# Kernel optimization log

Hardware: AMD Instinct MI355X
Metric: run time of the kernel (lower is better)

## Reference

```python
import jax, jax.numpy as jnp
import numpy as np

B, S, D, H = 4, 2048, 1024, 16
HD = D // H
BITS = 8
LEVELS = 2 ** BITS - 1          # number of negative log2 levels
SCALING = 32.0 / 16.0           # lora alpha / rank for 8-bit adapter
NEG_INF = -1e9


def log_fake_quant(x, reduce_axes):
    """Per-channel log-domain fake quantization with straight-through estimator.
    Scale = per-channel max-abs; magnitudes snapped to power-of-two fractions of scale."""
    s = jnp.maximum(jnp.max(jnp.abs(x), axis=reduce_axes, keepdims=True), 1e-8)
    ratio = jnp.clip(jnp.abs(x) / s, 2.0 ** (-LEVELS), 1.0)
    e = jnp.round(jnp.log2(ratio))                      # in [-LEVELS, 0]
    q = jnp.sign(x) * s * jnp.exp2(e)
    return x + jax.lax.stop_gradient(q - x)             # STE


def cpt_linear(x, W, b, lA, lB):
    """CPTLinear: fake-quantized activation/weight GEMM + bias + LoRA on the fp input."""
    xq = log_fake_quant(x, tuple(range(x.ndim - 1)))     # per last-dim channel
    Wq = log_fake_quant(W, (1,))                         # per output row (channel_dim=0)
    out = xq @ Wq.T + b
    return out + (x @ lA @ lB) * SCALING


def setup_inputs() -> dict:
    key = jax.random.key(0)
    ks = jax.random.split(key, 8)
    causal = jnp.tril(jnp.ones((S, S), dtype=bool))
    mask = jnp.where(causal, 0.0, NEG_INF).astype(jnp.float32)[None, None]  # [1,1,S,S]
    return {
        "hidden_states": jax.random.normal(ks[0], (B, S, D), jnp.float32),
        "attention_mask": mask,
        "W_attn": jax.random.normal(ks[1], (3 * D, D), jnp.float32) * 0.02,
        "b_attn": jnp.zeros((3 * D,), jnp.float32),
        "lA_attn": jax.random.normal(ks[2], (D, 16), jnp.float32) * 0.01,
        "lB_attn": jax.random.normal(ks[3], (16, 3 * D), jnp.float32) * 0.01,
        "W_proj": jax.random.normal(ks[4], (D, D), jnp.float32) * 0.02,
        "b_proj": jnp.zeros((D,), jnp.float32),
        "lA_proj": jax.random.normal(ks[5], (D, 16), jnp.float32) * 0.01,
        "lB_proj": jax.random.normal(ks[6], (16, D), jnp.float32) * 0.01,
    }


def reference(hidden_states, attention_mask, W_attn, b_attn, lA_attn, lB_attn,
              W_proj, b_proj, lA_proj, lB_proj):
    qkv = cpt_linear(hidden_states, W_attn, b_attn, lA_attn, lB_attn)  # [B,S,3D]
    q, k, v = jnp.split(qkv, 3, axis=-1)

    def to_heads(t):
        return t.reshape(B, S, H, HD).transpose(0, 2, 1, 3)            # [B,H,S,HD]

    q, k, v = to_heads(q), to_heads(k), to_heads(v)
    scores = jnp.einsum("bhqd,bhkd->bhqk", q, k) / np.float32(np.sqrt(HD))
    scores = scores + attention_mask
    attn = jax.nn.softmax(scores, axis=-1)                             # dropout: eval mode (identity)
    out = jnp.einsum("bhqk,bhkd->bhqd", attn, v)
    out = out.transpose(0, 2, 1, 3).reshape(B, S, D)
    return cpt_linear(out, W_proj, b_proj, lA_proj, lB_proj)
```

## Files before the change

kernel.cpp:

```cpp
#include <hip/hip_runtime.h>

#define SS 2048
#define DD 1024
#define DQKV 3072
#define KP 1088
#define NT64 17
#define MTOT 8192
#define QKSZ ((size_t)MTOT * DD)

typedef unsigned short us;
typedef __attribute__((ext_vector_type(8))) short bf16x8;
typedef __attribute__((ext_vector_type(4))) float f32x4;
typedef __attribute__((ext_vector_type(4))) unsigned u32x4;

#define WAITVM(N) asm volatile("s_waitcnt vmcnt(" #N ")" ::: "memory")
#define WAITLGKM0 asm volatile("s_waitcnt lgkmcnt(0)" ::: "memory")

__device__ __forceinline__ us f2bf(float f) {
    unsigned u = __float_as_uint(f);
    return (us)((u + 0x7fffu + ((u >> 16) & 1u)) >> 16);
}
__device__ __forceinline__ float bf2f(us h) { return __uint_as_float(((unsigned)h) << 16); }
__device__ __forceinline__ void split2(float q, us& h, us& l) {
    h = f2bf(q); l = f2bf(q - bf2f(h));
}
__device__ __forceinline__ unsigned cvtpk(float lo, float hi) {
    unsigned r;
    asm("v_cvt_pk_bf16_f32 %0, %1, %2" : "=v"(r) : "v"(lo), "v"(hi));
    return r;
}

__device__ __forceinline__ int logq_e(float ax, float s) {
    int e = 0;
    if (ax < s) {
        double r = (double)ax / (double)s;
        int ex;
        double mant = frexp(r, &ex);
        e = (mant >= 0.70710678118654752440) ? ex : ex - 1;
        e = (e < -255) ? -255 : e;
    }
    return e;
}
__device__ __forceinline__ float logq_exact(float x, float s) {
    float ax = fabsf(x);
    if (ax == 0.f) return copysignf(0.f, x);
    return copysignf(ldexpf(s, logq_e(ax, s)), x);
}

__device__ __forceinline__ void gll16(const void* g, void* l) {
    __builtin_amdgcn_global_load_lds(
        (const __attribute__((address_space(1))) void*)g,
        (__attribute__((address_space(3))) void*)l, 16, 0, 0);
}


__global__ void k_zero(unsigned* p, int n) {
    int i = blockIdx.x * 256 + threadIdx.x;
    if (i < n) p[i] = 0u;
}

__global__ void k_colmax(const float* __restrict__ x, unsigned* __restrict__ smax) {
    int c = blockIdx.x * 256 + threadIdx.x;
    int r0 = blockIdx.y * 128;
    float m = 0.f;
    for (int r = 0; r < 128; ++r) m = fmaxf(m, fabsf(x[(size_t)(r0 + r) * DD + c]));
    atomicMax(smax + c, __float_as_uint(m));
}

__global__ void k_quant_rows(const float* __restrict__ x, const unsigned* __restrict__ smax,
                             us* __restrict__ xq) {
    int m = blockIdx.x, tx = threadIdx.x;
    float4 xv = ((const float4*)(x + (size_t)m * DD))[tx];
    int c = tx * 4;
    float vv[4] = {xv.x, xv.y, xv.z, xv.w};
    ushort4 qh;
    us* ph = (us*)&qh;
#pragma unroll
    for (int j = 0; j < 4; ++j) {
        float s = fmaxf(__uint_as_float(smax[c + j]), 1e-8f);
        float sh = bf2f(f2bf(s));
        float ax = fabsf(vv[j]);
        if (ax == 0.f) ph[j] = (us)((__float_as_uint(vv[j]) >> 16) & 0x8000u);
        else ph[j] = f2bf(copysignf(ldexpf(sh, logq_e(ax, s)), vv[j]));
    }
    *(ushort4*)(xq + (size_t)m * KP + c) = qh;
    if (tx == 0) xq[(size_t)m * KP + 1056] = 0x3F80;
    else if (tx < 32) xq[(size_t)m * KP + 1056 + tx] = 0;
}

__global__ void k_lora_x(const float* __restrict__ x, const float* __restrict__ lA,
                         us* __restrict__ xq) {
    int w = threadIdx.x >> 6, lane = threadIdx.x & 63;
    int m = blockIdx.x * 4 + w;
    const float* xr = x + (size_t)m * DD;
    float acc[16];
#pragma unroll
    for (int r = 0; r < 16; ++r) acc[r] = 0.f;
#pragma unroll
    for (int i = 0; i < 4; ++i) {
        int c0 = i * 256 + lane * 4;
        float4 xv = *(const float4*)(xr + c0);
        float xs4[4] = {xv.x, xv.y, xv.z, xv.w};
#pragma unroll
        for (int j = 0; j < 4; ++j) {
            float xs = xs4[j];
            const float4* lr = (const float4*)(lA + (size_t)(c0 + j) * 16);
            float4 a0 = lr[0], a1 = lr[1], a2 = lr[2], a3 = lr[3];
            acc[0] += xs * a0.x; acc[1] += xs * a0.y; acc[2] += xs * a0.z; acc[3] += xs * a0.w;
            acc[4] += xs * a1.x; acc[5] += xs * a1.y; acc[6] += xs * a1.z; acc[7] += xs * a1.w;
            acc[8] += xs * a2.x; acc[9] += xs * a2.y; acc[10] += xs * a2.z; acc[11] += xs * a2.w;
            acc[12] += xs * a3.x; acc[13] += xs * a3.y; acc[14] += xs * a3.z; acc[15] += xs * a3.w;
        }
    }
#pragma unroll
    for (int msk = 1; msk < 64; msk <<= 1)
#pragma unroll
        for (int r = 0; r < 16; ++r) acc[r] += __shfl_xor(acc[r], msk);
    if (lane == 0) {
#pragma unroll
        for (int r = 0; r < 16; ++r) {
            us h, l; split2(2.0f * acc[r], h, l);
            xq[(size_t)m * KP + 1024 + r] = h;
            xq[(size_t)m * KP + 1040 + r] = l;
        }
    }
}

__global__ __launch_bounds__(256) void k_quant_w(const float* __restrict__ W, const float* __restrict__ lB,
                                                 const float* __restrict__ bias,
                                                 const unsigned* __restrict__ smax,
                                                 us* __restrict__ wh, us* __restrict__ wl, int Nn) {
    __shared__ float red[4];
    int n = blockIdx.x, tx = threadIdx.x;
    int lane = tx & 63, w = tx >> 6;
    float4 wv = ((const float4*)(W + (size_t)n * DD))[tx];
    float m4 = fmaxf(fmaxf(fabsf(wv.x), fabsf(wv.y)), fmaxf(fabsf(wv.z), fabsf(wv.w)));
#pragma unroll
    for (int msk = 1; msk < 64; msk <<= 1) m4 = fmaxf(m4, __shfl_xor(m4, msk));
    if (lane == 0) red[w] = m4;
    __syncthreads();
    float t = fmaxf(fmaxf(fmaxf(red[0], red[1]), fmaxf(red[2], red[3])), 1e-8f);
    float vv[4] = {wv.x, wv.y, wv.z, wv.w};
    int c = tx * 4;
    ushort4 qh, ql;
    us* ph = (us*)&qh; us* pl = (us*)&ql;
#pragma unroll
    for (int j = 0; j < 4; ++j) {
        float s = fmaxf(__uint_as_float(smax[c + j]), 1e-8f);
        float sh = bf2f(f2bf(s));
        float rho = (s - sh) / sh;
        float q = logq_exact(vv[j], t);
        float wp = q + q * rho;
        split2(wp, ph[j], pl[j]);
    }
    *(ushort4*)(wh + (size_t)n * KP + c) = qh;
    *(ushort4*)(wl + (size_t)n * KP + c) = ql;
    if (tx < 64) {
        us h = 0, l = 0;
        if (tx < 32) { int r = tx & 15; split2(lB[(size_t)r * Nn + n], h, l); }
        else if (tx == 32) split2(bias[n], h, l);
        wh[(size_t)n * KP + 1024 + tx] = h;
        wl[(size_t)n * KP + 1024 + tx] = l;
    }
}


template <int MODE>
__global__ __launch_bounds__(512, 2) void k_gemm(const us* __restrict__ Aq_,
                                                 const us* __restrict__ Bh_, const us* __restrict__ Bl_,
                                                 float* __restrict__ C, int Nn,
                                                 us* __restrict__ Khg, us* __restrict__ Klg,
                                                 float* __restrict__ vbuf) {
    __shared__ us LA[2][16384];
    __shared__ us LBh[2][8192];
    __shared__ us LBl[2][8192];
    int tid = threadIdx.x;
    int bm = blockIdx.x, bn = blockIdx.y;
    int lane = tid & 63, w = tid >> 6;
    int wm = w >> 2, wn = w & 3;
    int l15 = lane & 15, l4 = lane >> 4;
    int srow = tid >> 3;
    int gsrc = ((tid & 7) ^ (srow & 7)) * 8;
    const us* aP  = Aq_ + (size_t)(bm * 256 + srow) * KP + gsrc;
    const us* bhP = Bh_ + (size_t)(bn * 128 + srow) * KP + gsrc;
    const us* blP = Bl_ + (size_t)(bn * 128 + srow) * KP + gsrc;
    f32x4 zero4 = {0.f, 0.f, 0.f, 0.f};
    f32x4 acc[8][2];
#pragma unroll
    for (int i = 0; i < 8; ++i) { acc[i][0] = zero4; acc[i][1] = zero4; }

#define GSTAGE(buf, kt)                                               \
    do {                                                              \
        int k0_ = (kt) * 64;                                          \
        gll16(aP + k0_,                    &LA[(buf)][0]     + tid * 8); \
        gll16(aP + (size_t)64  * KP + k0_, &LA[(buf)][4096]  + tid * 8); \
        gll16(aP + (size_t)128 * KP + k0_, &LA[(buf)][8192]  + tid * 8); \
        gll16(aP + (size_t)192 * KP + k0_, &LA[(buf)][12288] + tid * 8); \
        gll16(bhP + k0_,                   &LBh[(buf)][0]    + tid * 8); \
        gll16(bhP + (size_t)64 * KP + k0_, &LBh[(buf)][4096] + tid * 8); \
        gll16(blP + k0_,                   &LBl[(buf)][0]    + tid * 8); \
        gll16(blP + (size_t)64 * KP + k0_, &LBl[(buf)][4096] + tid * 8); \
    } while (0)

    GSTAGE(0, 0);
    GSTAGE(1, 1);
    WAITVM(8);
    __builtin_amdgcn_s_barrier();
    __builtin_amdgcn_sched_barrier(0);

    int gsw0 = ((l4)     ^ (l15 & 7)) * 8;
    int gsw1 = ((4 + l4) ^ (l15 & 7)) * 8;
    int cur = 0;
    for (int kt = 0; kt < NT64; ++kt) {
        const us* A0  = &LA[cur][0];
        const us* Bh0 = &LBh[cur][0];
        const us* Bl0 = &LBl[cur][0];
        bf16x8 a0[8], b0h[2], b0l[2];
#pragma unroll
        for (int i = 0; i < 8; ++i)
            a0[i] = *(const bf16x8*)(A0 + (wm * 128 + i * 16 + l15) * 64 + gsw0);
#pragma unroll
        for (int i = 0; i < 2; ++i) {
            b0h[i] = *(const bf16x8*)(Bh0 + (wn * 32 + i * 16 + l15) * 64 + gsw0);
            b0l[i] = *(const bf16x8*)(Bl0 + (wn * 32 + i * 16 + l15) * 64 + gsw0);
        }
        __builtin_amdgcn_s_setprio(1);
#pragma unroll
        for (int mi = 0; mi < 8; ++mi)
#pragma unroll
            for (int ni = 0; ni < 2; ++ni) {
                acc[mi][ni] = __builtin_amdgcn_mfma_f32_16x16x32_bf16(a0[mi], b0h[ni], acc[mi][ni], 0, 0, 0);
                acc[mi][ni] = __builtin_amdgcn_mfma_f32_16x16x32_bf16(a0[mi], b0l[ni], acc[mi][ni], 0, 0, 0);
            }
        __builtin_amdgcn_s_setprio(0);
        bf16x8 a1[8], b1h[2], b1l[2];
#pragma unroll
        for (int i = 0; i < 8; ++i)
            a1[i] = *(const bf16x8*)(A0 + (wm * 128 + i * 16 + l15) * 64 + gsw1);
#pragma unroll
        for (int i = 0; i < 2; ++i) {
            b1h[i] = *(const bf16x8*)(Bh0 + (wn * 32 + i * 16 + l15) * 64 + gsw1);
            b1l[i] = *(const bf16x8*)(Bl0 + (wn * 32 + i * 16 + l15) * 64 + gsw1);
        }
        WAITLGKM0;
        __builtin_amdgcn_sched_barrier(0);
        __builtin_amdgcn_s_barrier();
        __builtin_amdgcn_sched_barrier(0);
        if (kt + 2 < NT64) GSTAGE(cur, kt + 2);
        __builtin_amdgcn_s_setprio(1);
#pragma unroll
        for (int mi = 0; mi < 8; ++mi)
#pragma unroll
            for (int ni = 0; ni < 2; ++ni) {
                acc[mi][ni] = __builtin_amdgcn_mfma_f32_16x16x32_bf16(a1[mi], b1h[ni], acc[mi][ni], 0, 0, 0);
                acc[mi][ni] = __builtin_amdgcn_mfma_f32_16x16x32_bf16(a1[mi], b1l[ni], acc[mi][ni], 0, 0, 0);
            }
        __builtin_amdgcn_s_setprio(0);
        if (kt + 2 < NT64) { WAITVM(8); } else { WAITVM(0); }
        __builtin_amdgcn_s_barrier();
        __builtin_amdgcn_sched_barrier(0);
        cur ^= 1;
    }
#undef GSTAGE

    int plane = bn >> 3;
#pragma unroll
    for (int mi = 0; mi < 8; ++mi) {
#pragma unroll
        for (int ni = 0; ni < 2; ++ni) {
            int ncol = bn * 128 + wn * 32 + ni * 16 + l15;
            size_t mbase = (size_t)bm * 256 + wm * 128 + mi * 16 + l4 * 4;
#pragma unroll
            for (int rr = 0; rr < 4; ++rr) {
                float v = acc[mi][ni][rr];
                size_t m = mbase + rr;
                if (MODE == 0) {
                    C[m * (size_t)Nn + ncol] = v;
                } else {
                    int cc = ncol & 1023;
                    if (plane == 0) {
                        C[m * DD + cc] = v;
                    } else if (plane == 2) {
                        vbuf[m * DD + cc] = v;
                    } else {
                        us hh, ll; split2(v, hh, ll);
                        size_t d = ((size_t)((m >> 11) * 16 + (cc >> 6)) * SS + (m & 2047)) * 64 + (cc & 63);
                        Khg[d] = hh; Klg[d] = ll;
                    }
                }
            }
        }
    }
}


__global__ __launch_bounds__(256) void k_transpose_v(const float* __restrict__ vbuf,
                                                     us* __restrict__ vth, us* __restrict__ vtl) {
    __shared__ us th[64][72], tl[64][72];
    int st = blockIdx.x, bh = blockIdx.y;
    int bb = bh >> 4, h = bh & 15;
    int s0 = st * 64, tid = threadIdx.x;
    int sl = tid >> 2, c0 = (tid & 3) * 16;
    const float* src = vbuf + (size_t)(bb * SS + s0 + sl) * DD + h * 64 + c0;
#pragma unroll
    for (int j4 = 0; j4 < 4; ++j4) {
        float4 v = *(const float4*)(src + j4 * 4);
        float vv[4] = {v.x, v.y, v.z, v.w};
#pragma unroll
        for (int j = 0; j < 4; ++j) {
            us hh, ll; split2(vv[j], hh, ll);
            th[c0 + j4 * 4 + j][sl] = hh;
            tl[c0 + j4 * 4 + j][sl] = ll;
        }
    }
    __syncthreads();
#pragma unroll
    for (int p = 0; p < 2; ++p) {
        int gidx = p * 256 + tid;
        int hd = gidx >> 3, g = gidx & 7;
        int base = (g >> 2) * 32 + (g & 3) * 4;
        ushort4 a, b2, c, d2;
        a.x = th[hd][base];      a.y = th[hd][base + 1];  a.z = th[hd][base + 2];  a.w = th[hd][base + 3];
        b2.x = th[hd][base + 16]; b2.y = th[hd][base + 17]; b2.z = th[hd][base + 18]; b2.w = th[hd][base + 19];
        c.x = tl[hd][base];      c.y = tl[hd][base + 1];  c.z = tl[hd][base + 2];  c.w = tl[hd][base + 3];
        d2.x = tl[hd][base + 16]; d2.y = tl[hd][base + 17]; d2.z = tl[hd][base + 18]; d2.w = tl[hd][base + 19];
        size_t dof = ((size_t)bh * 64 + hd) * SS + s0 + g * 8;
        *(ushort4*)(vth + dof) = a;  *(ushort4*)(vth + dof + 4) = b2;
        *(ushort4*)(vtl + dof) = c;  *(ushort4*)(vtl + dof + 4) = d2;
    }
}


#define SCL 0.18033688011112042f

__global__ __launch_bounds__(256, 2) void k_attn(float* qo,
                                                 const us* __restrict__ Khg, const us* __restrict__ Klg,
                                                 const us* __restrict__ vth, const us* __restrict__ vtl) {
    __shared__ us L[2][16384];
    int bh = blockIdx.x;
    int qt = (int)(gridDim.y - 1) - blockIdx.y;
    int b = bh >> 4, h = bh & 15;
    int q0 = qt * 128;
    int tid = threadIdx.x, w = tid >> 6, lane = tid & 63;
    int l15 = lane & 15, l4 = lane >> 4;
    int qw = q0 + w * 32;
    int swz = l15 & 7;

    bf16x8 qh[2][2], ql[2][2];
#pragma unroll
    for (int qb = 0; qb < 2; ++qb)
#pragma unroll
        for (int hf = 0; hf < 2; ++hf) {
            const float* qp = qo + (size_t)(b * SS + qw + qb * 16 + l15) * DD + h * 64 + hf * 32 + l4 * 8;
            float4 a = *(const float4*)qp;
            float4 c = *(const float4*)(qp + 4);
            float vv[8] = {a.x, a.y, a.z, a.w, c.x, c.y, c.z, c.w};
            bf16x8 hq, lq;
#pragma unroll
            for (int j = 0; j < 8; ++j) {
                us hh = f2bf(vv[j]);
                hq[j] = (short)hh;
                lq[j] = (short)f2bf(vv[j] - bf2f(hh));
            }
            qh[qb][hf] = hq; ql[qb][hf] = lq;
        }

    f32x4 zero4 = {0.f, 0.f, 0.f, 0.f};
    f32x4 of[2][4];
#pragma unroll
    for (int i = 0; i < 2; ++i)
#pragma unroll
        for (int j = 0; j < 4; ++j) of[i][j] = zero4;
    float mrow[2] = {-1e30f, -1e30f}, lrow[2] = {0.f, 0.f};

    int r0 = tid >> 3, sl0 = (tid & 7) ^ (r0 & 7);
    int g1 = tid + 256, r1 = g1 >> 3, sl1 = (g1 & 7) ^ (r1 & 7);
    int koff0 = (bh * SS + r0) * 64 + sl0 * 8;
    int koff1 = (bh * SS + r1) * 64 + sl1 * 8;
    int voff0 = (bh * 64 + r0) * SS + sl0 * 8;
    int voff1 = (bh * 64 + r1) * SS + sl1 * 8;

    int ntiles = qt * 2 + 2;

#define STAGE(buf, tt)                                           \
    do {                                                         \
        int kv_ = (tt) * 64;                                     \
        us* D_ = &L[(buf)][0];                                   \
        int kadd_ = kv_ << 6;                                    \
        gll16(Khg + koff0 + kadd_, D_ + tid * 8);                \
        gll16(Khg + koff1 + kadd_, D_ + 2048 + tid * 8);         \
        gll16(Klg + koff0 + kadd_, D_ + 4096 + tid * 8);         \
        gll16(Klg + koff1 + kadd_, D_ + 6144 + tid * 8);         \
        gll16(vth + voff0 + kv_, D_ + 8192 + tid * 8);           \
        gll16(vth + voff1 + kv_, D_ + 10240 + tid * 8);          \
        gll16(vtl + voff0 + kv_, D_ + 12288 + tid * 8);          \
        gll16(vtl + voff1 + kv_, D_ + 14336 + tid * 8);          \
    } while (0)

    STAGE(0, 0);
    STAGE(1, 1);
    int cur = 0;

    for (int t = 0; t < ntiles; ++t) {
        int kv0 = t * 64;
        if (t + 1 < ntiles) WAITVM(8); else WAITVM(0);
        __builtin_amdgcn_s_barrier();

        if (kv0 <= qw + 31) {
            const us* Lc = &L[cur][0];

            f32x4 sf[4][2];
#pragma unroll
            for (int i = 0; i < 4; ++i) { sf[i][0] = zero4; sf[i][1] = zero4; }
            __builtin_amdgcn_s_setprio(1);
#pragma unroll
            for (int kb = 0; kb < 4; ++kb) {
                int rbase = (kb * 16 + l15) * 64;
#pragma unroll
                for (int hf = 0; hf < 2; ++hf) {
                    int off = rbase + (((hf * 4 + l4) ^ swz) * 8);
                    bf16x8 kh = *(const bf16x8*)(Lc + off);
                    bf16x8 kl = *(const bf16x8*)(Lc + 4096 + off);
#pragma unroll
                    for (int qb = 0; qb < 2; ++qb) {
                        sf[kb][qb] = __builtin_amdgcn_mfma_f32_16x16x32_bf16(kh, qh[qb][hf], sf[kb][qb], 0, 0, 0);
                        sf[kb][qb] = __builtin_amdgcn_mfma_f32_16x16x32_bf16(kh, ql[qb][hf], sf[kb][qb], 0, 0, 0);
                        sf[kb][qb] = __builtin_amdgcn_mfma_f32_16x16x32_bf16(kl, qh[qb][hf], sf[kb][qb], 0, 0, 0);
                    }
                }
            }
            __builtin_amdgcn_s_setprio(0);

            bool diag = (kv0 + 63 > qw);
            u32x4 PH[2][2], PL[2][2];
#pragma unroll
            for (int qb = 0; qb < 2; ++qb) {
                float pv[16];
                if (diag) {
                    int qg = qw + qb * 16 + l15;
#pragma unroll
                    for (int kb = 0; kb < 4; ++kb)
#pragma unroll
                        for (int rr = 0; rr < 4; ++rr) {
                            int kvg = kv0 + kb * 16 + l4 * 4 + rr;
                            float sc = sf[kb][qb][rr] * SCL;
                            pv[kb * 4 + rr] = (kvg > qg) ? -1e30f : sc;
                        }
                } else {
#pragma unroll
                    for (int kb = 0; kb < 4; ++kb)
#pragma unroll
                        for (int rr = 0; rr < 4; ++rr)
                            pv[kb * 4 + rr] = sf[kb][qb][rr] * SCL;
                }
                float tmax = pv[0];
#pragma unroll
                for (int i = 1; i < 16; ++i) tmax = fmaxf(tmax, pv[i]);
                tmax = fmaxf(tmax, __shfl_xor(tmax, 16));
                tmax = fmaxf(tmax, __shfl_xor(tmax, 32));
                float mnew = fmaxf(mrow[qb], tmax);
                float fac = __builtin_amdgcn_exp2f(mrow[qb] - mnew);
                mrow[qb] = mnew;
                float ps = 0.f;
#pragma unroll
                for (int i = 0; i < 16; ++i) {
                    pv[i] = __builtin_amdgcn_exp2f(pv[i] - mnew);
                    ps += pv[i];
                }
                ps += __shfl_xor(ps, 16); ps += __shfl_xor(ps, 32);
                lrow[qb] = lrow[qb] * fac + ps;
#pragma unroll
                for (int ks = 0; ks < 2; ++ks)
#pragma unroll
                    for (int c2 = 0; c2 < 4; ++c2) {
                        float p0 = pv[ks * 8 + c2 * 2], p1 = pv[ks * 8 + c2 * 2 + 1];
                        unsigned u = cvtpk(p0, p1);
                        float h0 = __uint_as_float(u << 16);
                        float h1 = __uint_as_float(u & 0xffff0000u);
                        unsigned ul = cvtpk(p0 - h0, p1 - h1);
                        PH[qb][ks][c2] = u; PL[qb][ks][c2] = ul;
                    }
                float fr0 = __shfl(fac, l4 * 4 + 0);
                float fr1 = __shfl(fac, l4 * 4 + 1);
                float fr2 = __shfl(fac, l4 * 4 + 2);
                float fr3 = __shfl(fac, l4 * 4 + 3);
#pragma unroll
                for (int hb = 0; hb < 4; ++hb) {
                    of[qb][hb][0] *= fr0; of[qb][hb][1] *= fr1;
                    of[qb][hb][2] *= fr2; of[qb][hb][3] *= fr3;
                }
            }

            __builtin_amdgcn_s_setprio(1);
#pragma unroll
            for (int hb = 0; hb < 4; ++hb) {
                int rbase = (hb * 16 + l15) * 64;
#pragma unroll
                for (int ks = 0; ks < 2; ++ks) {
                    int off = rbase + (((ks * 4 + l4) ^ swz) * 8);
                    bf16x8 vh = *(const bf16x8*)(Lc + 8192 + off);
                    bf16x8 vl = *(const bf16x8*)(Lc + 12288 + off);
#pragma unroll
                    for (int qb = 0; qb < 2; ++qb) {
                        bf16x8 pa = (bf16x8)PH[qb][ks];
                        bf16x8 pb = (bf16x8)PL[qb][ks];
                        of[qb][hb] = __builtin_amdgcn_mfma_f32_16x16x32_bf16(pa, vh, of[qb][hb], 0, 0, 0);
                        of[qb][hb] = __builtin_amdgcn_mfma_f32_16x16x32_bf16(pa, vl, of[qb][hb], 0, 0, 0);
                        of[qb][hb] = __builtin_amdgcn_mfma_f32_16x16x32_bf16(pb, vh, of[qb][hb], 0, 0, 0);
                    }
                }
            }
            __builtin_amdgcn_s_setprio(0);
        }

        __builtin_amdgcn_s_barrier();
        if (t + 2 < ntiles) STAGE(cur, t + 2);
        cur ^= 1;
    }
#undef STAGE

#pragma unroll
    for (int qb = 0; qb < 2; ++qb) {
        float linv = 1.f / lrow[qb];
        float f0 = __shfl(linv, l4 * 4 + 0);
        float f1 = __shfl(linv, l4 * 4 + 1);
        float f2 = __shfl(linv, l4 * 4 + 2);
        float f3 = __shfl(linv, l4 * 4 + 3);
        int qgb = qw + qb * 16 + l4 * 4;
#pragma unroll
        for (int hb = 0; hb < 4; ++hb) {
            int col = h * 64 + hb * 16 + l15;
            qo[((size_t)(b * SS + qgb + 0)) * DD + col] = of[qb][hb][0] * f0;
            qo[((size_t)(b * SS + qgb + 1)) * DD + col] = of[qb][hb][1] * f1;
            qo[((size_t)(b * SS + qgb + 2)) * DD + col] = of[qb][hb][2] * f2;
            qo[((size_t)(b * SS + qgb + 3)) * DD + col] = of[qb][hb][3] * f3;
        }
    }
}


extern "C" void kernel_launch(void* const* d_in, const int* in_sizes, int n_in,
                              void* d_out, int out_size, void* d_ws, size_t ws_size,
                              hipStream_t stream) {
    const float* hidden  = (const float*)d_in[0];
    const float* W_attn  = (const float*)d_in[2];
    const float* b_attn  = (const float*)d_in[3];
    const float* lA_attn = (const float*)d_in[4];
    const float* lB_attn = (const float*)d_in[5];
    const float* W_proj  = (const float*)d_in[6];
    const float* b_proj  = (const float*)d_in[7];
    const float* lA_proj = (const float*)d_in[8];
    const float* lB_proj = (const float*)d_in[9];
    float* out = (float*)d_out;

    char* ws = (char*)d_ws;
    unsigned* s1 = (unsigned*)(ws);
    unsigned* s2 = (unsigned*)(ws + 4096);
    us* xq  = (us*)(ws + 8192);
    us* vth = xq;
    us* wh1 = (us*)(ws + 8192 + 17825792);
    us* wl1 = (us*)(ws + 8192 + 17825792 + 6684672);
    us* wh2 = (us*)(ws + 8192 + 17825792 + 2 * 6684672);
    us* wl2 = (us*)(ws + 8192 + 17825792 + 2 * 6684672 + 2228224);
    char* pbase = ws + 8192 + 17825792 + 2 * 6684672 + 2 * 2228224;
    float* qbuf = (float*)pbase;
    float* vbuf = (float*)(pbase + 33554432);
    us* Khg = (us*)(pbase + 2 * (size_t)33554432);
    us* Klg = (us*)(pbase + 2 * (size_t)33554432 + 16777216);
    us* vtl = (us*)(pbase + 2 * (size_t)33554432 + 2 * (size_t)16777216);

    k_zero<<<8, 256, 0, stream>>>(s1, 2048);

    k_colmax<<<dim3(4, 64), 256, 0, stream>>>(hidden, s1);
    k_quant_rows<<<MTOT, 256, 0, stream>>>(hidden, s1, xq);
    k_lora_x<<<MTOT / 4, 256, 0, stream>>>(hidden, lA_attn, xq);
    k_quant_w<<<3072, 256, 0, stream>>>(W_attn, lB_attn, b_attn, s1, wh1, wl1, 3072);
    k_gemm<1><<<dim3(32, 24), 512, 0, stream>>>(xq, wh1, wl1, qbuf, DQKV, Khg, Klg, vbuf);

    k_transpose_v<<<dim3(32, 64), 256, 0, stream>>>(vbuf, vth, vtl);
    k_attn<<<dim3(64, 16), 256, 0, stream>>>(qbuf, Khg, Klg, vth, vtl);

    k_colmax<<<dim3(4, 64), 256, 0, stream>>>(qbuf, s2);
    k_quant_rows<<<MTOT, 256, 0, stream>>>(qbuf, s2, xq);
    k_lora_x<<<MTOT / 4, 256, 0, stream>>>(qbuf, lA_proj, xq);
    k_quant_w<<<1024, 256, 0, stream>>>(W_proj, lB_proj, b_proj, s2, wh2, wl2, 1024);
    k_gemm<0><<<dim3(32, 8), 512, 0, stream>>>(xq, wh2, wl2, out, DD, nullptr, nullptr, nullptr);
}
```

Baseline: 473.1 us.

## Fuse row quant with LoRA projection and lazily rescale attention softmax

Merges the activation quantization kernel and the LoRA down-projection kernel into one, so each row of the input is read once and one launch is dropped, twice per forward. Folds the softmax scale into K when the QKV GEMM writes it, removing a multiply per score. The flash-attention loop now rescales the running max and output accumulators only when some row's max grows by more than a threshold, and defers the cross-lane reduction of the row sum to the epilogue. This cuts shuffles and multiplies in the inner loop, at the cost of a wave-wide vote and a branch. It also slightly changes rounding, because K is scaled before the bf16 hi/lo split.

```diff
diff --git a/kernel.cpp b/kernel.cpp
--- a/kernel.cpp
+++ b/kernel.cpp
@@ -7,6 +7,7 @@
 #define NT64 17
 #define MTOT 8192
 #define QKSZ ((size_t)MTOT * DD)
+#define SCL 0.18033688011112042f
 
 typedef unsigned short us;
 typedef __attribute__((ext_vector_type(8))) short bf16x8;
@@ -67,9 +68,13 @@
     atomicMax(smax + c, __float_as_uint(m));
 }
 
-__global__ void k_quant_rows(const float* __restrict__ x, const unsigned* __restrict__ smax,
-                             us* __restrict__ xq) {
+__global__ __launch_bounds__(256) void k_quant_lora(const float* __restrict__ x,
+                                                    const unsigned* __restrict__ smax,
+                                                    const float* __restrict__ lA,
+                                                    us* __restrict__ xq) {
+    __shared__ float red[4][16];
     int m = blockIdx.x, tx = threadIdx.x;
+    int lane = tx & 63, w = tx >> 6;
     float4 xv = ((const float4*)(x + (size_t)m * DD))[tx];
     int c = tx * 4;
     float vv[4] = {xv.x, xv.y, xv.z, xv.w};
@@ -84,45 +89,36 @@
         else ph[j] = f2bf(copysignf(ldexpf(sh, logq_e(ax, s)), vv[j]));
     }
     *(ushort4*)(xq + (size_t)m * KP + c) = qh;
-    if (tx == 0) xq[(size_t)m * KP + 1056] = 0x3F80;
-    else if (tx < 32) xq[(size_t)m * KP + 1056 + tx] = 0;
-}
-
-__global__ void k_lora_x(const float* __restrict__ x, const float* __restrict__ lA,
-                         us* __restrict__ xq) {
-    int w = threadIdx.x >> 6, lane = threadIdx.x & 63;
-    int m = blockIdx.x * 4 + w;
-    const float* xr = x + (size_t)m * DD;
     float acc[16];
 #pragma unroll
     for (int r = 0; r < 16; ++r) acc[r] = 0.f;
 #pragma unroll
-    for (int i = 0; i < 4; ++i) {
-        int c0 = i * 256 + lane * 4;
-        float4 xv = *(const float4*)(xr + c0);
-        float xs4[4] = {xv.x, xv.y, xv.z, xv.w};
-#pragma unroll
-        for (int j = 0; j < 4; ++j) {
-            float xs = xs4[j];
-            const float4* lr = (const float4*)(lA + (size_t)(c0 + j) * 16);
-            float4 a0 = lr[0], a1 = lr[1], a2 = lr[2], a3 = lr[3];
-            acc[0] += xs * a0.x; acc[1] += xs * a0.y; acc[2] += xs * a0.z; acc[3] += xs * a0.w;
-            acc[4] += xs * a1.x; acc[5] += xs * a1.y; acc[6] += xs * a1.z; acc[7] += xs * a1.w;
-            acc[8] += xs * a2.x; acc[9] += xs * a2.y; acc[10] += xs * a2.z; acc[11] += xs * a2.w;
-            acc[12] += xs * a3.x; acc[13] += xs * a3.y; acc[14] += xs * a3.z; acc[15] += xs * a3.w;
-        }
+    for (int j = 0; j < 4; ++j) {
+        float xs = vv[j];
+        const float4* lr = (const float4*)(lA + (size_t)(c + j) * 16);
+        float4 a0 = lr[0], a1 = lr[1], a2 = lr[2], a3 = lr[3];
+        acc[0] += xs * a0.x; acc[1] += xs * a0.y; acc[2] += xs * a0.z; acc[3] += xs * a0.w;
+        acc[4] += xs * a1.x; acc[5] += xs * a1.y; acc[6] += xs * a1.z; acc[7] += xs * a1.w;
+        acc[8] += xs * a2.x; acc[9] += xs * a2.y; acc[10] += xs * a2.z; acc[11] += xs * a2.w;
+        acc[12] += xs * a3.x; acc[13] += xs * a3.y; acc[14] += xs * a3.z; acc[15] += xs * a3.w;
     }
 #pragma unroll
     for (int msk = 1; msk < 64; msk <<= 1)
 #pragma unroll
         for (int r = 0; r < 16; ++r) acc[r] += __shfl_xor(acc[r], msk);
-    if (lane == 0) {
-#pragma unroll
-        for (int r = 0; r < 16; ++r) {
-            us h, l; split2(2.0f * acc[r], h, l);
-            xq[(size_t)m * KP + 1024 + r] = h;
-            xq[(size_t)m * KP + 1040 + r] = l;
-        }
+    if (lane == 0)
+#pragma unroll
+        for (int r = 0; r < 16; ++r) red[w][r] = acc[r];
+    __syncthreads();
+    if (tx < 16) {
+        float v = 2.0f * (red[0][tx] + red[1][tx] + red[2][tx] + red[3][tx]);
+        us h, l; split2(v, h, l);
+        xq[(size_t)m * KP + 1024 + tx] = h;
+        xq[(size_t)m * KP + 1040 + tx] = l;
+    } else if (tx == 16) {
+        xq[(size_t)m * KP + 1056] = 0x3F80;
+    } else if (tx < 48) {
+        xq[(size_t)m * KP + 1040 + tx] = 0;
     }
 }
 
@@ -283,7 +279,7 @@
                     } else if (plane == 2) {
                         vbuf[m * DD + cc] = v;
                     } else {
-                        us hh, ll; split2(v, hh, ll);
+                        us hh, ll; split2(v * SCL, hh, ll);
                         size_t d = ((size_t)((m >> 11) * 16 + (cc >> 6)) * SS + (m & 2047)) * 64 + (cc & 63);
                         Khg[d] = hh; Klg[d] = ll;
                     }
@@ -331,8 +327,6 @@
 }
 
 
-#define SCL 0.18033688011112042f
-
 __global__ __launch_bounds__(256, 2) void k_attn(float* qo,
                                                  const us* __restrict__ Khg, const us* __restrict__ Klg,
                                                  const us* __restrict__ vth, const us* __restrict__ vtl) {
@@ -371,7 +365,7 @@
     for (int i = 0; i < 2; ++i)
 #pragma unroll
         for (int j = 0; j < 4; ++j) of[i][j] = zero4;
-    float mrow[2] = {-1e30f, -1e30f}, lrow[2] = {0.f, 0.f};
+    float mrow[2] = {-1e30f, -1e30f}, lrowp[2] = {0.f, 0.f};
 
     int r0 = tid >> 3, sl0 = (tid & 7) ^ (r0 & 7);
     int g1 = tid + 256, r1 = g1 >> 3, sl1 = (g1 & 7) ^ (r1 & 7);
@@ -443,32 +437,46 @@
 #pragma unroll
                         for (int rr = 0; rr < 4; ++rr) {
                             int kvg = kv0 + kb * 16 + l4 * 4 + rr;
-                            float sc = sf[kb][qb][rr] * SCL;
-                            pv[kb * 4 + rr] = (kvg > qg) ? -1e30f : sc;
+                            pv[kb * 4 + rr] = (kvg > qg) ? -1e30f : sf[kb][qb][rr];
                         }
                 } else {
 #pragma unroll
                     for (int kb = 0; kb < 4; ++kb)
 #pragma unroll
                         for (int rr = 0; rr < 4; ++rr)
-                            pv[kb * 4 + rr] = sf[kb][qb][rr] * SCL;
+                            pv[kb * 4 + rr] = sf[kb][qb][rr];
                 }
-                float tmax = pv[0];
-#pragma unroll
-                for (int i = 1; i < 16; ++i) tmax = fmaxf(tmax, pv[i]);
+                float t0 = fmaxf(fmaxf(pv[0], pv[1]), pv[2]);
+                float t1 = fmaxf(fmaxf(pv[3], pv[4]), pv[5]);
+                float t2 = fmaxf(fmaxf(pv[6], pv[7]), pv[8]);
+                float t3 = fmaxf(fmaxf(pv[9], pv[10]), pv[11]);
+                float t4 = fmaxf(fmaxf(pv[12], pv[13]), pv[14]);
+                float tmax = fmaxf(fmaxf(fmaxf(t0, t1), fmaxf(t2, t3)), fmaxf(t4, pv[15]));
                 tmax = fmaxf(tmax, __shfl_xor(tmax, 16));
                 tmax = fmaxf(tmax, __shfl_xor(tmax, 32));
-                float mnew = fmaxf(mrow[qb], tmax);
-                float fac = __builtin_amdgcn_exp2f(mrow[qb] - mnew);
-                mrow[qb] = mnew;
+                float mcur = mrow[qb];
+                if (!__all(tmax <= mcur + 8.0f)) {
+                    float mnew = fmaxf(mcur, tmax);
+                    float fac = __builtin_amdgcn_exp2f(mcur - mnew);
+                    mrow[qb] = mnew; mcur = mnew;
+                    lrowp[qb] *= fac;
+                    float fr0 = __shfl(fac, l4 * 4 + 0);
+                    float fr1 = __shfl(fac, l4 * 4 + 1);
+                    float fr2 = __shfl(fac, l4 * 4 + 2);
+                    float fr3 = __shfl(fac, l4 * 4 + 3);
+#pragma unroll
+                    for (int hb = 0; hb < 4; ++hb) {
+                        of[qb][hb][0] *= fr0; of[qb][hb][1] *= fr1;
+                        of[qb][hb][2] *= fr2; of[qb][hb][3] *= fr3;
+                    }
+                }
                 float ps = 0.f;
 #pragma unroll
                 for (int i = 0; i < 16; ++i) {
-                    pv[i] = __builtin_amdgcn_exp2f(pv[i] - mnew);
+                    pv[i] = __builtin_amdgcn_exp2f(pv[i] - mcur);
                     ps += pv[i];
                 }
-                ps += __shfl_xor(ps, 16); ps += __shfl_xor(ps, 32);
-                lrow[qb] = lrow[qb] * fac + ps;
+                lrowp[qb] += ps;
 #pragma unroll
                 for (int ks = 0; ks < 2; ++ks)
 #pragma unroll
@@ -480,15 +488,6 @@
                         unsigned ul = cvtpk(p0 - h0, p1 - h1);
                         PH[qb][ks][c2] = u; PL[qb][ks][c2] = ul;
                     }
-                float fr0 = __shfl(fac, l4 * 4 + 0);
-                float fr1 = __shfl(fac, l4 * 4 + 1);
-                float fr2 = __shfl(fac, l4 * 4 + 2);
-                float fr3 = __shfl(fac, l4 * 4 + 3);
-#pragma unroll
-                for (int hb = 0; hb < 4; ++hb) {
-                    of[qb][hb][0] *= fr0; of[qb][hb][1] *= fr1;
-                    of[qb][hb][2] *= fr2; of[qb][hb][3] *= fr3;
-                }
             }
 
             __builtin_amdgcn_s_setprio(1);
@@ -521,7 +520,10 @@
 
 #pragma unroll
     for (int qb = 0; qb < 2; ++qb) {
-        float linv = 1.f / lrow[qb];
+        float lr = lrowp[qb];
+        lr += __shfl_xor(lr, 16);
+        lr += __shfl_xor(lr, 32);
+        float linv = 1.f / lr;
         float f0 = __shfl(linv, l4 * 4 + 0);
         float f1 = __shfl(linv, l4 * 4 + 1);
         float f2 = __shfl(linv, l4 * 4 + 2);
@@ -572,8 +574,7 @@
     k_zero<<<8, 256, 0, stream>>>(s1, 2048);
 
     k_colmax<<<dim3(4, 64), 256, 0, stream>>>(hidden, s1);
-    k_quant_rows<<<MTOT, 256, 0, stream>>>(hidden, s1, xq);
-    k_lora_x<<<MTOT / 4, 256, 0, stream>>>(hidden, lA_attn, xq);
+    k_quant_lora<<<MTOT, 256, 0, stream>>>(hidden, s1, lA_attn, xq);
     k_quant_w<<<3072, 256, 0, stream>>>(W_attn, lB_attn, b_attn, s1, wh1, wl1, 3072);
     k_gemm<1><<<dim3(32, 24), 512, 0, stream>>>(xq, wh1, wl1, qbuf, DQKV, Khg, Klg, vbuf);
 
@@ -581,8 +582,7 @@
     k_attn<<<dim3(64, 16), 256, 0, stream>>>(qbuf, Khg, Klg, vth, vtl);
 
     k_colmax<<<dim3(4, 64), 256, 0, stream>>>(qbuf, s2);
-    k_quant_rows<<<MTOT, 256, 0, stream>>>(qbuf, s2, xq);
-    k_lora_x<<<MTOT / 4, 256, 0, stream>>>(qbuf, lA_proj, xq);
+    k_quant_lora<<<MTOT, 256, 0, stream>>>(qbuf, s2, lA_proj, xq);
     k_quant_w<<<1024, 256, 0, stream>>>(W_proj, lB_proj, b_proj, s2, wh2, wl2, 1024);
     k_gemm<0><<<dim3(32, 8), 512, 0, stream>>>(xq, wh2, wl2, out, DD, nullptr, nullptr, nullptr);
 }
```

After: 450.7 us. -4.7%, faster.
